# Performance work log

Hardware: AMD Instinct MI355X
Metric: run time of the kernel (lower is better)

The kernel has to match this reference:

```python
import jax, jax.numpy as jnp
import numpy as np

B, T, C, H, R = 2, 2048, 2048, 16, 8
D = C // H  # head_dim = 128


def _rope_cache(seq_len, dim, theta=10000.0):
    pos = jnp.arange(seq_len, dtype=jnp.float32)[:, None]            # [T,1]
    idx = jnp.arange(0, dim, 2, dtype=jnp.float32)                   # [D/2]
    freqs = 1.0 / (theta ** (idx / dim))
    ang = pos * freqs                                                # [T, D/2]
    return jnp.cos(ang), jnp.sin(ang)


def setup_inputs() -> dict:
    key = jax.random.key(0)
    ks = jax.random.split(key, 16)
    s = 0.02
    inp = {"x": jax.random.normal(ks[0], (B, T, C), dtype=jnp.float32)}
    i = 1
    for nm in ("q", "k", "v", "p"):
        inp[f"{nm}_w"] = jax.random.normal(ks[i], (C, C), dtype=jnp.float32) * s; i += 1
        inp[f"{nm}_b"] = jnp.zeros((C,), dtype=jnp.float32)
        inp[f"{nm}_A"] = jax.random.normal(ks[i], (C, R), dtype=jnp.float32) * s; i += 1
        inp[f"{nm}_B"] = jax.random.normal(ks[i], (R, C), dtype=jnp.float32) * s; i += 1
    cos, sin = _rope_cache(T, D)
    inp["cos"] = cos
    inp["sin"] = sin
    inp["mask"] = jnp.tril(jnp.ones((T, T), dtype=bool))  # causal SDPA mask
    inp["use_lora"] = 1
    return inp


def _lora_linear(x, w, b, A, Bm, use_lora):
    # base GEMM + bias, plus low-rank adapter x @ A @ B (intended path)
    out = x @ w.T + b
    if use_lora:
        out = out + (x @ A) @ Bm
    return out


def _apply_rope(x, cos, sin):
    # x: [B,H,T,D]; cos/sin: [T, D/2] broadcast over batch & heads
    x1 = x[..., ::2]
    x2 = x[..., 1::2]
    y = jnp.stack((x1 * cos - x2 * sin, x1 * sin + x2 * cos), axis=-1)
    return y.reshape(x.shape)


def reference(x, q_w, q_b, q_A, q_B, k_w, k_b, k_A, k_B,
              v_w, v_b, v_A, v_B, p_w, p_b, p_A, p_B,
              cos, sin, mask, use_lora):
    Bsz, Tl, Cd = x.shape
    q = _lora_linear(x, q_w, q_b, q_A, q_B, use_lora).reshape(Bsz, Tl, H, D).transpose(0, 2, 1, 3)
    k = _lora_linear(x, k_w, k_b, k_A, k_B, use_lora).reshape(Bsz, Tl, H, D).transpose(0, 2, 1, 3)
    v = _lora_linear(x, v_w, v_b, v_A, v_B, use_lora).reshape(Bsz, Tl, H, D).transpose(0, 2, 1, 3)
    q = _apply_rope(q, cos, sin)
    k = _apply_rope(k, cos, sin)
    # scaled dot-product attention with boolean mask (True = attend)
    scale = 1.0 / jnp.sqrt(jnp.asarray(D, dtype=x.dtype))
    scores = jnp.einsum('bhqd,bhkd->bhqk', q, k) * scale          # [B,H,T,T]
    neg = jnp.asarray(jnp.finfo(scores.dtype).min, dtype=scores.dtype)
    scores = jnp.where(mask, scores, neg)
    attn = jax.nn.softmax(scores, axis=-1)
    out = jnp.einsum('bhqk,bhkd->bhqd', attn, v)                  # [B,H,T,D]
    y = out.transpose(0, 2, 1, 3).reshape(Bsz, Tl, Cd)
    return _lora_linear(y, p_w, p_b, p_A, p_B, use_lora)
```

## Files before the change

### kernel.cpp

```cpp
#include <hip/hip_runtime.h>

typedef _Float16 f16;
typedef _Float16 f16x4 __attribute__((ext_vector_type(4)));
typedef _Float16 f16x8 __attribute__((ext_vector_type(8)));
typedef __fp16 hf2 __attribute__((ext_vector_type(2)));
typedef float f32x4 __attribute__((ext_vector_type(4)));

#define DEV static __device__ __forceinline__

DEV void gl_lds16(const void* g, void* l) {
  __builtin_amdgcn_global_load_lds(
      (const __attribute__((address_space(1))) void*)g,
      (__attribute__((address_space(3))) void*)l, 16, 0, 0);
}

DEV uint pkrtz(float a, float b) {
  hf2 h = __builtin_amdgcn_cvt_pkrtz(a, b);
  return __builtin_bit_cast(uint, h);
}

__global__ void cast_f16_kernel(const float* __restrict__ x,
                                const float* __restrict__ w0,
                                const float* __restrict__ w1,
                                const float* __restrict__ w2,
                                const float* __restrict__ w3,
                                f16* __restrict__ xb, f16* __restrict__ b0,
                                f16* __restrict__ b1, f16* __restrict__ b2,
                                f16* __restrict__ b3) {
  const int total4 = (8388608 + 4 * 4194304) / 4;
  for (int i = blockIdx.x * blockDim.x + threadIdx.x; i < total4;
       i += gridDim.x * blockDim.x) {
    int e = i << 2;
    const float* s; f16* d; int off;
    if (e < 8388608)        { s = x;  d = xb; off = e; }
    else if (e < 12582912)  { s = w0; d = b0; off = e - 8388608; }
    else if (e < 16777216)  { s = w1; d = b1; off = e - 12582912; }
    else if (e < 20971520)  { s = w2; d = b2; off = e - 16777216; }
    else                    { s = w3; d = b3; off = e - 20971520; }
    float4 v = *(const float4*)(s + off);
    f16x4 hv = {(f16)v.x, (f16)v.y, (f16)v.z, (f16)v.w};
    *(f16x4*)(d + off) = hv;
  }
}

__global__ __launch_bounds__(256) void lora_x_kernel(
    const float* __restrict__ x, const float* __restrict__ Aq,
    const float* __restrict__ Ak, const float* __restrict__ Av,
    float* __restrict__ la) {
  const int wave = threadIdx.x >> 6, lane = threadIdx.x & 63;
  const int m = blockIdx.x * 4 + wave;
  const float* xrow = x + (size_t)m * 2048;
  const float* As[3] = {Aq, Ak, Av};
  float acc[3][8] = {};
  for (int i = 0; i < 32; ++i) {
    int k = i * 64 + lane;
    float xv = xrow[k];
#pragma unroll
    for (int nm = 0; nm < 3; ++nm) {
      const float4* ap = (const float4*)(As[nm] + (size_t)k * 8);
      float4 a0 = ap[0], a1 = ap[1];
      acc[nm][0] += xv * a0.x; acc[nm][1] += xv * a0.y;
      acc[nm][2] += xv * a0.z; acc[nm][3] += xv * a0.w;
      acc[nm][4] += xv * a1.x; acc[nm][5] += xv * a1.y;
      acc[nm][6] += xv * a1.z; acc[nm][7] += xv * a1.w;
    }
  }
#pragma unroll
  for (int nm = 0; nm < 3; ++nm)
#pragma unroll
    for (int r = 0; r < 8; ++r) {
      float v = acc[nm][r];
#pragma unroll
      for (int off = 1; off < 64; off <<= 1) v += __shfl_xor(v, off);
      acc[nm][r] = v;
    }
  if (lane == 0) {
#pragma unroll
    for (int nm = 0; nm < 3; ++nm)
#pragma unroll
      for (int r = 0; r < 8; ++r)
        la[nm * 32768 + (size_t)m * 8 + r] = acc[nm][r];
  }
}

__global__ __launch_bounds__(256) void lora_p_kernel(
    const f16* __restrict__ y, const float* __restrict__ Ap,
    float* __restrict__ lap) {
  const int wave = threadIdx.x >> 6, lane = threadIdx.x & 63;
  const int m = blockIdx.x * 4 + wave;
  const f16* yrow = y + (size_t)m * 2048;
  float acc[8] = {};
  for (int i = 0; i < 4; ++i) {
    int k0 = i * 512 + lane * 8;
    f16x8 yv = *(const f16x8*)(yrow + k0);
#pragma unroll
    for (int j = 0; j < 8; ++j) {
      float xv = (float)yv[j];
      const float4* ap = (const float4*)(Ap + (size_t)(k0 + j) * 8);
      float4 a0 = ap[0], a1 = ap[1];
      acc[0] += xv * a0.x; acc[1] += xv * a0.y;
      acc[2] += xv * a0.z; acc[3] += xv * a0.w;
      acc[4] += xv * a1.x; acc[5] += xv * a1.y;
      acc[6] += xv * a1.z; acc[7] += xv * a1.w;
    }
  }
#pragma unroll
  for (int r = 0; r < 8; ++r) {
    float v = acc[r];
#pragma unroll
    for (int off = 1; off < 64; off <<= 1) v += __shfl_xor(v, off);
    acc[r] = v;
  }
  if (lane == 0) {
#pragma unroll
    for (int r = 0; r < 8; ++r) lap[(size_t)m * 8 + r] = acc[r];
  }
}

template <int MODE>
__global__ __launch_bounds__(256, 2) void gemm_kernel(
    const f16* __restrict__ A, const f16* __restrict__ Bw,
    const float* __restrict__ bias, const float* __restrict__ la,
    const float* __restrict__ Bm, const int* __restrict__ use_lora,
    const float* __restrict__ cosT, const float* __restrict__ sinT,
    void* __restrict__ out) {
  __shared__ char smem[32768];
  const int tid = threadIdx.x;
  const int wave = tid >> 6, lane = tid & 63;
  const int lr = lane & 15, lg = lane >> 4;
  const int bm = blockIdx.x >> 4, bn = blockIdx.x & 15;
  const int m0 = bm << 7, n0 = bn << 7;
  const int wr = wave >> 1, wc = wave & 1;

  uint aoff[4], boff[4];
#pragma unroll
  for (int r = 0; r < 4; ++r) {
    uint beta = (uint)(wave * 4 + r) * 1024 + (uint)lane * 16;
    uint row = beta >> 7;
    uint c = (beta & 127u) ^ ((row & 7u) << 4);
    aoff[r] = (uint)(m0 + row) * 4096 + c;
    boff[r] = (uint)(n0 + row) * 4096 + c;
  }
  const char* Ab = (const char*)A;
  const char* Bb = (const char*)Bw;

  f32x4 acc[4][4] = {};

  for (int kt = 0; kt < 32; ++kt) {
    __syncthreads();
    const int kb = kt << 7;
#pragma unroll
    for (int r = 0; r < 4; ++r) {
      gl_lds16(Ab + (size_t)(aoff[r] + kb), smem + (wave * 4 + r) * 1024);
      gl_lds16(Bb + (size_t)(boff[r] + kb), smem + 16384 + (wave * 4 + r) * 1024);
    }
    __syncthreads();

    f16x8 af[2][4], bf[2][4];
#pragma unroll
    for (int ks = 0; ks < 2; ++ks) {
#pragma unroll
      for (int mi = 0; mi < 4; ++mi) {
        int row = wr * 64 + mi * 16 + lr;
        int c = (ks * 64 + lg * 16) ^ ((row & 7) << 4);
        af[ks][mi] = *(const f16x8*)(smem + row * 128 + c);
      }
#pragma unroll
      for (int ni = 0; ni < 4; ++ni) {
        int row = wc * 64 + ni * 16 + lr;
        int c = (ks * 64 + lg * 16) ^ ((row & 7) << 4);
        bf[ks][ni] = *(const f16x8*)(smem + 16384 + row * 128 + c);
      }
    }
    __builtin_amdgcn_s_setprio(1);
#pragma unroll
    for (int ks = 0; ks < 2; ++ks)
#pragma unroll
      for (int mi = 0; mi < 4; ++mi)
#pragma unroll
        for (int ni = 0; ni < 4; ++ni)
          acc[mi][ni] = __builtin_amdgcn_mfma_f32_16x16x32_f16(
              af[ks][mi], bf[ks][ni], acc[mi][ni], 0, 0, 0);
    __builtin_amdgcn_s_setprio(0);
  }

  const int ul = use_lora[0];
  __syncthreads();

  float bv[4], bml[4][8];
#pragma unroll
  for (int ni = 0; ni < 4; ++ni) {
    int n = n0 + wc * 64 + ni * 16 + lr;
    bv[ni] = bias[n];
    if (ul) {
#pragma unroll
      for (int r = 0; r < 8; ++r) bml[ni][r] = Bm[r * 2048 + n];
    }
  }

  f16* stg = (f16*)smem;
#pragma unroll
  for (int mi = 0; mi < 4; ++mi) {
    const int mbase = m0 + wr * 64 + mi * 16 + lg * 4;
    float lar[4][8];
    if (ul) {
#pragma unroll
      for (int rg = 0; rg < 4; ++rg) {
        const float4* lp = (const float4*)(la + (size_t)(mbase + rg) * 8);
        float4 l0 = lp[0], l1 = lp[1];
        lar[rg][0] = l0.x; lar[rg][1] = l0.y; lar[rg][2] = l0.z; lar[rg][3] = l0.w;
        lar[rg][4] = l1.x; lar[rg][5] = l1.y; lar[rg][6] = l1.z; lar[rg][7] = l1.w;
      }
    }
#pragma unroll
    for (int ni = 0; ni < 4; ++ni) {
      const int n = n0 + wc * 64 + ni * 16 + lr;
#pragma unroll
      for (int rg = 0; rg < 4; ++rg) {
        float v = acc[mi][ni][rg] + bv[ni];
        if (ul) {
#pragma unroll
          for (int r = 0; r < 8; ++r) v += lar[rg][r] * bml[ni][r];
        }
        if (MODE == 0) {
          float pv = __shfl_xor(v, 1);
          const int m = mbase + rg;
          const int t = m & 2047;
          const int d = n & 127;
          const int ci = t * 64 + (d >> 1);
          float cs = cosT[ci], sn = sinT[ci];
          float res = ((lane & 1) == 0) ? (v * cs - pv * sn)
                                        : (pv * sn + v * cs);
          stg[(wr * 64 + mi * 16 + lg * 4 + rg) * 128 +
              (wc * 64 + ni * 16 + lr)] = (f16)res;
        } else if (MODE == 1) {
          stg[(wr * 64 + mi * 16 + lg * 4 + rg) * 128 +
              (wc * 64 + ni * 16 + lr)] = (f16)v;
        } else {
          ((float*)out)[(size_t)(mbase + rg) * 2048 + n] = v;
        }
      }
    }
  }

  if (MODE < 2) {
    __syncthreads();
    if (MODE == 0) {
      const long b_ = m0 >> 11;
      const int tb = m0 & 2047;
      char* obase = (char*)out + ((b_ * 16 + bn) * 2048 + tb) * 256;
#pragma unroll
      for (int p = 0; p < 8; ++p) {
        int s = p * 4096 + tid * 16;
        int row = s >> 8, c = s & 255;
        *(uint4*)(obase + (long)row * 256 + c) = *(const uint4*)(smem + s);
      }
    } else {
      char* obase = (char*)out + ((long)m0 * 2048 + n0) * 2;
#pragma unroll
      for (int p = 0; p < 8; ++p) {
        int s = p * 4096 + tid * 16;
        int row = s >> 8, c = s & 255;
        *(uint4*)(obase + (long)row * 4096 + c) = *(const uint4*)(smem + s);
      }
    }
  }
}

__global__ void transpose_v_kernel(const ushort* __restrict__ vbi,
                                   ushort* __restrict__ vto) {
  __shared__ ushort tile[32][33];
  const int t0 = blockIdx.x << 5;
  const int d0 = blockIdx.y << 5;
  const int bh = blockIdx.z;
  const int b = bh >> 4, h = bh & 15;
  const int tx = threadIdx.x, ty = threadIdx.y;
  const ushort* src = vbi + ((size_t)(b * 2048 + t0)) * 2048 + h * 128 + d0;
#pragma unroll
  for (int i = 0; i < 4; ++i)
    tile[ty + 8 * i][tx] = src[(size_t)(ty + 8 * i) * 2048 + tx];
  __syncthreads();
  ushort* dst = vto + ((size_t)bh * 128 + d0) * 2048 + t0;
#pragma unroll
  for (int i = 0; i < 4; ++i)
    dst[(size_t)(ty + 8 * i) * 2048 + tx] = tile[tx][ty + 8 * i];
}

__global__ __launch_bounds__(256, 2) void attn_kernel(
    const f16* __restrict__ qr, const f16* __restrict__ kr,
    const f16* __restrict__ vt, f16* __restrict__ y) {
  __shared__ char smem[32768];
  char* Ks = smem;
  char* Vs = smem + 16384;
  const int tid = threadIdx.x, wave = tid >> 6, lane = tid & 63;
  const int lr = lane & 15, lg = lane >> 4;
  const int qtile = 31 - (int)blockIdx.x;
  const int q0 = qtile << 6;
  const int h = blockIdx.y, b = blockIdx.z;
  const long bh = b * 16 + h;

  const char* qbase = (const char*)qr + (bh * 2048 + q0 + wave * 16 + lr) * 256;
  f16x8 qf[4];
#pragma unroll
  for (int ks = 0; ks < 4; ++ks)
    qf[ks] = *(const f16x8*)(qbase + ks * 64 + lg * 16);

  f32x4 o[8] = {};
  float mrow = -3e38f, lsum = 0.f;
  const int qa = q0 + wave * 16 + lr;

  const char* kbase = (const char*)kr + bh * 2048 * 256;
  const char* vbase = (const char*)vt + bh * 128 * 4096;
  const float SC2 = 0.12752551286084103f;

  for (int kt = 0; kt <= qtile; ++kt) {
    const int kv0 = kt << 6;
    __syncthreads();
#pragma unroll
    for (int r = 0; r < 4; ++r) {
      uint s = (uint)(wave * 4 + r) * 1024 + (uint)lane * 16;
      {
        uint row = s >> 8, c = (s & 255u) ^ ((row & 7u) << 4);
        gl_lds16(kbase + (size_t)(kv0 + row) * 256 + c,
                 Ks + (wave * 4 + r) * 1024);
      }
      {
        uint row = s >> 7, c = (s & 127u) ^ ((row & 7u) << 4);
        gl_lds16(vbase + (size_t)row * 4096 + kv0 * 2 + c,
                 Vs + (wave * 4 + r) * 1024);
      }
    }
    __syncthreads();

    f32x4 sa[4] = {};
    __builtin_amdgcn_s_setprio(1);
#pragma unroll
    for (int ks = 0; ks < 4; ++ks)
#pragma unroll
      for (int n = 0; n < 4; ++n) {
        int row = n * 16 + lr;
        int c = (ks * 64 + lg * 16) ^ ((row & 7) << 4);
        f16x8 kf = *(const f16x8*)(Ks + row * 256 + c);
        sa[n] = __builtin_amdgcn_mfma_f32_16x16x32_f16(kf, qf[ks], sa[n], 0, 0, 0);
      }
    __builtin_amdgcn_s_setprio(0);

    float L[16];
    float pm = -3e38f;
    const bool diag = (kt == qtile);
#pragma unroll
    for (int n = 0; n < 4; ++n)
#pragma unroll
      for (int rg = 0; rg < 4; ++rg) {
        float Lv = sa[n][rg] * SC2;
        if (diag && (kv0 + n * 16 + lg * 4 + rg > qa)) Lv = -3e37f;
        L[n * 4 + rg] = Lv;
        pm = fmaxf(pm, Lv);
      }
    pm = fmaxf(pm, __shfl_xor(pm, 16));
    pm = fmaxf(pm, __shfl_xor(pm, 32));
    float mn = fmaxf(mrow, pm);
    float alpha = exp2f(mrow - mn);
    mrow = mn;
    float ps = 0.f;
#pragma unroll
    for (int i = 0; i < 16; ++i) {
      float p = exp2f(L[i] - mn);
      L[i] = p;
      ps += p;
    }
    ps += __shfl_xor(ps, 16);
    ps += __shfl_xor(ps, 32);
    lsum = lsum * alpha + ps;
#pragma unroll
    for (int dt = 0; dt < 8; ++dt)
#pragma unroll
      for (int rg = 0; rg < 4; ++rg) o[dt][rg] *= alpha;

#pragma unroll
    for (int ks2 = 0; ks2 < 2; ++ks2) {
      uint w0 = pkrtz(L[8 * ks2 + 0], L[8 * ks2 + 1]);
      uint w1 = pkrtz(L[8 * ks2 + 2], L[8 * ks2 + 3]);
      uint w2 = pkrtz(L[8 * ks2 + 4], L[8 * ks2 + 5]);
      uint w3 = pkrtz(L[8 * ks2 + 6], L[8 * ks2 + 7]);
      int src1 = ((lg & 1) << 5) + lr;
      int src2 = src1 + 16;
      uint a0 = __shfl((int)w0, src1), a1 = __shfl((int)w1, src1);
      uint a2 = __shfl((int)w2, src1), a3 = __shfl((int)w3, src1);
      uint b0 = __shfl((int)w0, src2), b1 = __shfl((int)w1, src2);
      uint b2 = __shfl((int)w2, src2), b3 = __shfl((int)w3, src2);
      const bool hi = (lg >> 1) != 0;
      uint4 uu;
      uu.x = hi ? a2 : a0;
      uu.y = hi ? a3 : a1;
      uu.z = hi ? b2 : b0;
      uu.w = hi ? b3 : b1;
      f16x8 pf = __builtin_bit_cast(f16x8, uu);
      __builtin_amdgcn_s_setprio(1);
#pragma unroll
      for (int dt = 0; dt < 8; ++dt) {
        int drow = dt * 16 + lr;
        int c = (ks2 * 64 + lg * 16) ^ ((drow & 7) << 4);
        f16x8 vf = *(const f16x8*)(Vs + drow * 128 + c);
        o[dt] = __builtin_amdgcn_mfma_f32_16x16x32_f16(vf, pf, o[dt], 0, 0, 0);
      }
      __builtin_amdgcn_s_setprio(0);
    }
  }

  __syncthreads();
  const float inv = 1.f / lsum;
  {
    const int row = wave * 16 + lr;
#pragma unroll
    for (int dt = 0; dt < 8; ++dt) {
      uint lo = pkrtz(o[dt][0] * inv, o[dt][1] * inv);
      uint hi2 = pkrtz(o[dt][2] * inv, o[dt][3] * inv);
      int c = (dt * 32 + lg * 8) ^ ((row & 7) << 4);
      uint2 w; w.x = lo; w.y = hi2;
      *(uint2*)(smem + row * 256 + c) = w;
    }
  }
  __syncthreads();
#pragma unroll
  for (int p = 0; p < 4; ++p) {
    int s = p * 4096 + tid * 16;
    int row = s >> 8, cb = s & 255;
    int c = cb ^ ((row & 7) << 4);
    char* dst = (char*)y + ((long)(b * 2048 + q0 + row) * 2048 + h * 128) * 2 + cb;
    *(uint4*)dst = *(const uint4*)(smem + row * 256 + c);
  }
}

extern "C" void kernel_launch(void* const* d_in, const int* in_sizes, int n_in,
                              void* d_out, int out_size, void* d_ws,
                              size_t ws_size, hipStream_t stream) {
  (void)in_sizes; (void)n_in; (void)out_size; (void)ws_size;
  const float* x   = (const float*)d_in[0];
  const float* q_w = (const float*)d_in[1];
  const float* q_b = (const float*)d_in[2];
  const float* q_A = (const float*)d_in[3];
  const float* q_B = (const float*)d_in[4];
  const float* k_w = (const float*)d_in[5];
  const float* k_b = (const float*)d_in[6];
  const float* k_A = (const float*)d_in[7];
  const float* k_B = (const float*)d_in[8];
  const float* v_w = (const float*)d_in[9];
  const float* v_b = (const float*)d_in[10];
  const float* v_A = (const float*)d_in[11];
  const float* v_B = (const float*)d_in[12];
  const float* p_w = (const float*)d_in[13];
  const float* p_b = (const float*)d_in[14];
  const float* p_A = (const float*)d_in[15];
  const float* p_B = (const float*)d_in[16];
  const float* cosT = (const float*)d_in[17];
  const float* sinT = (const float*)d_in[18];
  const int* use_lora = (const int*)d_in[20];

  char* ws = (char*)d_ws;
  f16* xb  = (f16*)(ws);
  f16* wqb = (f16*)(ws + 16777216);
  f16* wkb = (f16*)(ws + 25165824);
  f16* wvb = (f16*)(ws + 33554432);
  f16* wpb = (f16*)(ws + 41943040);
  float* la = (float*)(ws + 50331648);
  f16* qr  = (f16*)(ws + 50855936);
  f16* kr  = (f16*)(ws + 67633152);
  f16* vb  = (f16*)(ws + 84410368);
  f16* vt  = (f16*)(ws);
  f16* y   = vb;
  float* lap = la + 98304;

  cast_f16_kernel<<<dim3(2048), dim3(256), 0, stream>>>(
      x, q_w, k_w, v_w, p_w, xb, wqb, wkb, wvb, wpb);
  lora_x_kernel<<<dim3(1024), dim3(256), 0, stream>>>(x, q_A, k_A, v_A, la);
  gemm_kernel<0><<<dim3(512), dim3(256), 0, stream>>>(
      xb, wqb, q_b, la, q_B, use_lora, cosT, sinT, (void*)qr);
  gemm_kernel<0><<<dim3(512), dim3(256), 0, stream>>>(
      xb, wkb, k_b, la + 32768, k_B, use_lora, cosT, sinT, (void*)kr);
  gemm_kernel<1><<<dim3(512), dim3(256), 0, stream>>>(
      xb, wvb, v_b, la + 65536, v_B, use_lora, nullptr, nullptr, (void*)vb);
  transpose_v_kernel<<<dim3(64, 4, 32), dim3(32, 8), 0, stream>>>(
      (const ushort*)vb, (ushort*)vt);
  attn_kernel<<<dim3(32, 16, 2), dim3(256), 0, stream>>>(qr, kr, vt, y);
  lora_p_kernel<<<dim3(1024), dim3(256), 0, stream>>>(y, p_A, lap);
  gemm_kernel<2><<<dim3(512), dim3(256), 0, stream>>>(
      y, wpb, p_b, lap, p_B, use_lora, nullptr, nullptr, d_out);
}
```

Before: 399.0 us.

## Double-buffer K/V in LDS and process 128-query tiles per block

The attention kernel now handles 128 query rows per block, with each wave computing two 16-row groups, so every K/V fragment read from LDS feeds two MFMAs. K/V tiles are double-buffered in 64 KB of dynamic LDS so the next tile's global-to-LDS load is issued before the current tile is computed, leaving one barrier per iteration. Waves whose rows lie entirely above the causal diagonal skip compute on that tile. In exchange, register pressure roughly doubles, the grid halves to 512 blocks, and the larger LDS footprint may lower occupancy.

```diff
diff --git a/kernel.cpp b/kernel.cpp
--- a/kernel.cpp
+++ b/kernel.cpp
@@ -289,145 +289,174 @@
 __global__ __launch_bounds__(256, 2) void attn_kernel(
     const f16* __restrict__ qr, const f16* __restrict__ kr,
     const f16* __restrict__ vt, f16* __restrict__ y) {
-  __shared__ char smem[32768];
-  char* Ks = smem;
-  char* Vs = smem + 16384;
+  extern __shared__ char smem[];
   const int tid = threadIdx.x, wave = tid >> 6, lane = tid & 63;
   const int lr = lane & 15, lg = lane >> 4;
-  const int qtile = 31 - (int)blockIdx.x;
-  const int q0 = qtile << 6;
+  const int qt = 15 - (int)blockIdx.x;
+  const int q0 = qt << 7;
   const int h = blockIdx.y, b = blockIdx.z;
   const long bh = b * 16 + h;
-
-  const char* qbase = (const char*)qr + (bh * 2048 + q0 + wave * 16 + lr) * 256;
-  f16x8 qf[4];
-#pragma unroll
-  for (int ks = 0; ks < 4; ++ks)
-    qf[ks] = *(const f16x8*)(qbase + ks * 64 + lg * 16);
-
-  f32x4 o[8] = {};
-  float mrow = -3e38f, lsum = 0.f;
-  const int qa = q0 + wave * 16 + lr;
+  const int nt = 2 * qt + 2;
 
   const char* kbase = (const char*)kr + bh * 2048 * 256;
   const char* vbase = (const char*)vt + bh * 128 * 4096;
+
+  f16x8 qf[2][4];
+#pragma unroll
+  for (int g = 0; g < 2; ++g) {
+    const char* qb =
+        (const char*)qr + (bh * 2048 + q0 + wave * 32 + g * 16 + lr) * 256;
+#pragma unroll
+    for (int ks = 0; ks < 4; ++ks)
+      qf[g][ks] = *(const f16x8*)(qb + ks * 64 + lg * 16);
+  }
+
+  f32x4 o[2][8] = {};
+  float mrow[2] = {-3e38f, -3e38f};
+  float lsum[2] = {0.f, 0.f};
   const float SC2 = 0.12752551286084103f;
 
-  for (int kt = 0; kt <= qtile; ++kt) {
-    const int kv0 = kt << 6;
-    __syncthreads();
+  auto STAGE = [&](int kv0, int bsel) {
+    char* Ks = smem + bsel * 32768;
+    char* Vs = Ks + 16384;
 #pragma unroll
     for (int r = 0; r < 4; ++r) {
       uint s = (uint)(wave * 4 + r) * 1024 + (uint)lane * 16;
-      {
-        uint row = s >> 8, c = (s & 255u) ^ ((row & 7u) << 4);
-        gl_lds16(kbase + (size_t)(kv0 + row) * 256 + c,
-                 Ks + (wave * 4 + r) * 1024);
-      }
-      {
-        uint row = s >> 7, c = (s & 127u) ^ ((row & 7u) << 4);
-        gl_lds16(vbase + (size_t)row * 4096 + kv0 * 2 + c,
-                 Vs + (wave * 4 + r) * 1024);
+      uint rowk = s >> 8, ck = (s & 255u) ^ ((rowk & 7u) << 4);
+      gl_lds16(kbase + (size_t)(kv0 + rowk) * 256 + ck,
+               Ks + (wave * 4 + r) * 1024);
+      uint rowv = s >> 7, cv = (s & 127u) ^ ((rowv & 7u) << 4);
+      gl_lds16(vbase + (size_t)rowv * 4096 + kv0 * 2 + cv,
+               Vs + (wave * 4 + r) * 1024);
+    }
+  };
+
+  STAGE(0, 0);
+  __syncthreads();
+
+  for (int kt = 0; kt < nt; ++kt) {
+    const int kv0 = kt << 6;
+    if (kt + 1 < nt) STAGE((kt + 1) << 6, (kt + 1) & 1);
+    const char* Ks = smem + (kt & 1) * 32768;
+    const char* Vs = Ks + 16384;
+
+    if (kv0 <= q0 + wave * 32 + 31) {
+      f32x4 sa[2][4] = {};
+      __builtin_amdgcn_s_setprio(1);
+#pragma unroll
+      for (int ks = 0; ks < 4; ++ks)
+#pragma unroll
+        for (int n = 0; n < 4; ++n) {
+          int row = n * 16 + lr;
+          int c = (ks * 64 + lg * 16) ^ ((row & 7) << 4);
+          f16x8 kf = *(const f16x8*)(Ks + row * 256 + c);
+          sa[0][n] =
+              __builtin_amdgcn_mfma_f32_16x16x32_f16(kf, qf[0][ks], sa[0][n], 0, 0, 0);
+          sa[1][n] =
+              __builtin_amdgcn_mfma_f32_16x16x32_f16(kf, qf[1][ks], sa[1][n], 0, 0, 0);
+        }
+      __builtin_amdgcn_s_setprio(0);
+
+      f16x8 pf[2][2];
+#pragma unroll
+      for (int g = 0; g < 2; ++g) {
+        const int qgbase = q0 + wave * 32 + g * 16;
+        float L[16];
+        float pm = -3e38f;
+        const bool dm = (kv0 + 63 > qgbase);
+#pragma unroll
+        for (int n = 0; n < 4; ++n)
+#pragma unroll
+          for (int rg = 0; rg < 4; ++rg) {
+            float Lv = sa[g][n][rg] * SC2;
+            if (dm && (kv0 + n * 16 + lg * 4 + rg > qgbase + lr)) Lv = -3e37f;
+            L[n * 4 + rg] = Lv;
+            pm = fmaxf(pm, Lv);
+          }
+        pm = fmaxf(pm, __shfl_xor(pm, 16));
+        pm = fmaxf(pm, __shfl_xor(pm, 32));
+        float mn = fmaxf(mrow[g], pm);
+        float alpha = exp2f(mrow[g] - mn);
+        mrow[g] = mn;
+        float ps = 0.f;
+#pragma unroll
+        for (int i = 0; i < 16; ++i) {
+          float p = exp2f(L[i] - mn);
+          L[i] = p;
+          ps += p;
+        }
+        ps += __shfl_xor(ps, 16);
+        ps += __shfl_xor(ps, 32);
+        lsum[g] = lsum[g] * alpha + ps;
+#pragma unroll
+        for (int dt = 0; dt < 8; ++dt)
+#pragma unroll
+          for (int rg = 0; rg < 4; ++rg) o[g][dt][rg] *= alpha;
+
+#pragma unroll
+        for (int ks2 = 0; ks2 < 2; ++ks2) {
+          uint w0 = pkrtz(L[8 * ks2 + 0], L[8 * ks2 + 1]);
+          uint w1 = pkrtz(L[8 * ks2 + 2], L[8 * ks2 + 3]);
+          uint w2 = pkrtz(L[8 * ks2 + 4], L[8 * ks2 + 5]);
+          uint w3 = pkrtz(L[8 * ks2 + 6], L[8 * ks2 + 7]);
+          int src1 = ((lg & 1) << 5) + lr;
+          int src2 = src1 + 16;
+          uint a0 = __shfl((int)w0, src1), a1 = __shfl((int)w1, src1);
+          uint a2 = __shfl((int)w2, src1), a3 = __shfl((int)w3, src1);
+          uint b0 = __shfl((int)w0, src2), b1 = __shfl((int)w1, src2);
+          uint b2 = __shfl((int)w2, src2), b3 = __shfl((int)w3, src2);
+          const bool hi = (lg >> 1) != 0;
+          uint4 uu;
+          uu.x = hi ? a2 : a0;
+          uu.y = hi ? a3 : a1;
+          uu.z = hi ? b2 : b0;
+          uu.w = hi ? b3 : b1;
+          pf[g][ks2] = __builtin_bit_cast(f16x8, uu);
+        }
+      }
+
+#pragma unroll
+      for (int ks2 = 0; ks2 < 2; ++ks2) {
+        __builtin_amdgcn_s_setprio(1);
+#pragma unroll
+        for (int dt = 0; dt < 8; ++dt) {
+          int drow = dt * 16 + lr;
+          int c = (ks2 * 64 + lg * 16) ^ ((drow & 7) << 4);
+          f16x8 vf = *(const f16x8*)(Vs + drow * 128 + c);
+          o[0][dt] =
+              __builtin_amdgcn_mfma_f32_16x16x32_f16(vf, pf[0][ks2], o[0][dt], 0, 0, 0);
+          o[1][dt] =
+              __builtin_amdgcn_mfma_f32_16x16x32_f16(vf, pf[1][ks2], o[1][dt], 0, 0, 0);
+        }
+        __builtin_amdgcn_s_setprio(0);
       }
     }
     __syncthreads();
-
-    f32x4 sa[4] = {};
-    __builtin_amdgcn_s_setprio(1);
-#pragma unroll
-    for (int ks = 0; ks < 4; ++ks)
-#pragma unroll
-      for (int n = 0; n < 4; ++n) {
-        int row = n * 16 + lr;
-        int c = (ks * 64 + lg * 16) ^ ((row & 7) << 4);
-        f16x8 kf = *(const f16x8*)(Ks + row * 256 + c);
-        sa[n] = __builtin_amdgcn_mfma_f32_16x16x32_f16(kf, qf[ks], sa[n], 0, 0, 0);
-      }
-    __builtin_amdgcn_s_setprio(0);
-
-    float L[16];
-    float pm = -3e38f;
-    const bool diag = (kt == qtile);
-#pragma unroll
-    for (int n = 0; n < 4; ++n)
-#pragma unroll
-      for (int rg = 0; rg < 4; ++rg) {
-        float Lv = sa[n][rg] * SC2;
-        if (diag && (kv0 + n * 16 + lg * 4 + rg > qa)) Lv = -3e37f;
-        L[n * 4 + rg] = Lv;
-        pm = fmaxf(pm, Lv);
-      }
-    pm = fmaxf(pm, __shfl_xor(pm, 16));
-    pm = fmaxf(pm, __shfl_xor(pm, 32));
-    float mn = fmaxf(mrow, pm);
-    float alpha = exp2f(mrow - mn);
-    mrow = mn;
-    float ps = 0.f;
-#pragma unroll
-    for (int i = 0; i < 16; ++i) {
-      float p = exp2f(L[i] - mn);
-      L[i] = p;
-      ps += p;
-    }
-    ps += __shfl_xor(ps, 16);
-    ps += __shfl_xor(ps, 32);
-    lsum = lsum * alpha + ps;
-#pragma unroll
-    for (int dt = 0; dt < 8; ++dt)
-#pragma unroll
-      for (int rg = 0; rg < 4; ++rg) o[dt][rg] *= alpha;
-
-#pragma unroll
-    for (int ks2 = 0; ks2 < 2; ++ks2) {
-      uint w0 = pkrtz(L[8 * ks2 + 0], L[8 * ks2 + 1]);
-      uint w1 = pkrtz(L[8 * ks2 + 2], L[8 * ks2 + 3]);
-      uint w2 = pkrtz(L[8 * ks2 + 4], L[8 * ks2 + 5]);
-      uint w3 = pkrtz(L[8 * ks2 + 6], L[8 * ks2 + 7]);
-      int src1 = ((lg & 1) << 5) + lr;
-      int src2 = src1 + 16;
-      uint a0 = __shfl((int)w0, src1), a1 = __shfl((int)w1, src1);
-      uint a2 = __shfl((int)w2, src1), a3 = __shfl((int)w3, src1);
-      uint b0 = __shfl((int)w0, src2), b1 = __shfl((int)w1, src2);
-      uint b2 = __shfl((int)w2, src2), b3 = __shfl((int)w3, src2);
-      const bool hi = (lg >> 1) != 0;
-      uint4 uu;
-      uu.x = hi ? a2 : a0;
-      uu.y = hi ? a3 : a1;
-      uu.z = hi ? b2 : b0;
-      uu.w = hi ? b3 : b1;
-      f16x8 pf = __builtin_bit_cast(f16x8, uu);
-      __builtin_amdgcn_s_setprio(1);
-#pragma unroll
-      for (int dt = 0; dt < 8; ++dt) {
-        int drow = dt * 16 + lr;
-        int c = (ks2 * 64 + lg * 16) ^ ((drow & 7) << 4);
-        f16x8 vf = *(const f16x8*)(Vs + drow * 128 + c);
-        o[dt] = __builtin_amdgcn_mfma_f32_16x16x32_f16(vf, pf, o[dt], 0, 0, 0);
-      }
-      __builtin_amdgcn_s_setprio(0);
-    }
-  }
-
+  }
+
+#pragma unroll
+  for (int g = 0; g < 2; ++g) {
+    const float inv = 1.f / lsum[g];
+    const int row = wave * 32 + g * 16 + lr;
+#pragma unroll
+    for (int dt = 0; dt < 8; ++dt) {
+      uint lo = pkrtz(o[g][dt][0] * inv, o[g][dt][1] * inv);
+      uint hi2 = pkrtz(o[g][dt][2] * inv, o[g][dt][3] * inv);
+      int c = (dt * 32 + lg * 8) ^ ((row & 7) << 4);
+      uint2 w;
+      w.x = lo;
+      w.y = hi2;
+      *(uint2*)(smem + row * 256 + c) = w;
+    }
+  }
   __syncthreads();
-  const float inv = 1.f / lsum;
-  {
-    const int row = wave * 16 + lr;
-#pragma unroll
-    for (int dt = 0; dt < 8; ++dt) {
-      uint lo = pkrtz(o[dt][0] * inv, o[dt][1] * inv);
-      uint hi2 = pkrtz(o[dt][2] * inv, o[dt][3] * inv);
-      int c = (dt * 32 + lg * 8) ^ ((row & 7) << 4);
-      uint2 w; w.x = lo; w.y = hi2;
-      *(uint2*)(smem + row * 256 + c) = w;
-    }
-  }
-  __syncthreads();
-#pragma unroll
-  for (int p = 0; p < 4; ++p) {
+#pragma unroll
+  for (int p = 0; p < 8; ++p) {
     int s = p * 4096 + tid * 16;
     int row = s >> 8, cb = s & 255;
     int c = cb ^ ((row & 7) << 4);
-    char* dst = (char*)y + ((long)(b * 2048 + q0 + row) * 2048 + h * 128) * 2 + cb;
+    char* dst =
+        (char*)y + ((long)(b * 2048 + q0 + row) * 2048 + h * 128) * 2 + cb;
     *(uint4*)dst = *(const uint4*)(smem + row * 256 + c);
   }
 }
@@ -482,7 +511,7 @@
       xb, wvb, v_b, la + 65536, v_B, use_lora, nullptr, nullptr, (void*)vb);
   transpose_v_kernel<<<dim3(64, 4, 32), dim3(32, 8), 0, stream>>>(
       (const ushort*)vb, (ushort*)vt);
-  attn_kernel<<<dim3(32, 16, 2), dim3(256), 0, stream>>>(qr, kr, vt, y);
+  attn_kernel<<<dim3(16, 16, 2), dim3(256), 65536, stream>>>(qr, kr, vt, y);
   lora_p_kernel<<<dim3(1024), dim3(256), 0, stream>>>(y, p_A, lap);
   gemm_kernel<2><<<dim3(512), dim3(256), 0, stream>>>(
       y, wpb, p_b, lap, p_B, use_lora, nullptr, nullptr, d_out);
```

Measured after the change: 393.4 us. Within noise of the previous version (-1.4%).
